# Kernel optimization log

Hardware: AMD Instinct MI355X
Metric: run time of the kernel (lower is better)

Reference implementation:

```python
import jax, jax.numpy as jnp
import numpy as np

HIDDEN = 768
NUM_HEADS = 12
HEAD_SIZE = HIDDEN // NUM_HEADS
LN_EPS = 1e-5


def setup_inputs() -> dict:
    key = jax.random.key(0)
    ks = jax.random.split(key, 10)
    B, S, H = 2, 4096, HIDDEN
    std = 1.0 / np.sqrt(H)
    inp = {
        "hidden_states": jax.random.normal(ks[0], (B, S, H), dtype=jnp.float32),
        "attention_mask": jnp.ones((B, S), dtype=jnp.float32),
        "Wq": jax.random.normal(ks[1], (H, H), dtype=jnp.float32) * std,
        "bq": jnp.zeros((H,), dtype=jnp.float32),
        "Wk": jax.random.normal(ks[2], (H, H), dtype=jnp.float32) * std,
        "bk": jnp.zeros((H,), dtype=jnp.float32),
        "Wv": jax.random.normal(ks[3], (H, H), dtype=jnp.float32) * std,
        "bv": jnp.zeros((H,), dtype=jnp.float32),
        "Wo": jax.random.normal(ks[4], (H, H), dtype=jnp.float32) * std,
        "bo": jnp.zeros((H,), dtype=jnp.float32),
        "ln_gamma": jnp.ones((H,), dtype=jnp.float32),
        "ln_beta": jnp.zeros((H,), dtype=jnp.float32),
    }
    return inp


def _split_heads(x):
    # [B, S, H] -> [B, nH, S, hd]
    B, S, _ = x.shape
    return x.reshape(B, S, NUM_HEADS, HEAD_SIZE).transpose(0, 2, 1, 3)


def reference(hidden_states, attention_mask, Wq, bq, Wk, bk, Wv, bv, Wo, bo, ln_gamma, ln_beta):
    # QKV projections (torch Linear: x @ W.T + b; here W is stored as [in, out])
    q = _split_heads(hidden_states @ Wq + bq)
    k = _split_heads(hidden_states @ Wk + bk)
    v = _split_heads(hidden_states @ Wv + bv)

    scores = jnp.einsum("bhqd,bhkd->bhqk", q, k) / jnp.sqrt(jnp.float32(HEAD_SIZE))
    # additive mask: (1 - mask) * -10000, broadcast over heads and query positions
    scores = scores + (1.0 - attention_mask)[:, None, None, :] * -10000.0
    probs = jax.nn.softmax(scores, axis=-1)  # dropout_prob = 0 -> identity

    ctx = jnp.einsum("bhqk,bhkd->bhqd", probs, v)
    B, _, S, _ = ctx.shape
    ctx = ctx.transpose(0, 2, 1, 3).reshape(B, S, HIDDEN)

    out = ctx @ Wo + bo
    resid = out + hidden_states
    mu = jnp.mean(resid, axis=-1, keepdims=True)
    var = jnp.var(resid, axis=-1, keepdims=True)
    return (resid - mu) * jax.lax.rsqrt(var + LN_EPS) * ln_gamma + ln_beta
```

## Files before the change

kernel.cpp:

```cpp
#include <hip/hip_runtime.h>
#include <hip/hip_bf16.h>

#define HID 768
#define NHEADS 12
#define HDIM 64
#define SEQ 4096
#define BB 2
#define MTOT (BB * SEQ)

typedef __attribute__((ext_vector_type(8))) short bf16x8;
typedef __attribute__((ext_vector_type(16))) float f32x16;

#define LOG2E 1.4426950408889634f

__device__ inline unsigned pack2bf(float a, float b) {
    __hip_bfloat162 h = __float22bfloat162_rn(float2{a, b});
    return *(unsigned*)&h;
}

__global__ __launch_bounds__(256) void cast_x_kernel(
    const float* __restrict__ X, __hip_bfloat16* __restrict__ Xb)
{
    const size_t i = ((size_t)blockIdx.x * 256 + threadIdx.x) * 8;
    const float4 x0 = *(const float4*)(X + i);
    const float4 x1 = *(const float4*)(X + i + 4);
    unsigned u[4];
    u[0] = pack2bf(x0.x, x0.y);
    u[1] = pack2bf(x0.z, x0.w);
    u[2] = pack2bf(x1.x, x1.y);
    u[3] = pack2bf(x1.z, x1.w);
    *(uint4*)(Xb + i) = *(uint4*)u;
}

__global__ __launch_bounds__(256) void pack_w_kernel(
    const float* __restrict__ Wq, const float* __restrict__ Wk,
    const float* __restrict__ Wv, const float* __restrict__ Wo,
    __hip_bfloat16* __restrict__ Wt)
{
    const int z = blockIdx.z;
    const float* __restrict__ W = (z == 0) ? Wq : (z == 1) ? Wk : (z == 2) ? Wv : Wo;
    const int in0  = blockIdx.x * 64;
    const int out0 = blockIdx.y * 64;
    const int t = threadIdx.x;

    __shared__ float T[64][65];
#pragma unroll
    for (int i = 0; i < 4; ++i) {
        const int idx = t + 256 * i;
        const int row = idx >> 4;
        const int c4  = (idx & 15) << 2;
        const float4 v = *(const float4*)(W + (size_t)(in0 + row) * HID + out0 + c4);
        T[row][c4 + 0] = v.x; T[row][c4 + 1] = v.y;
        T[row][c4 + 2] = v.z; T[row][c4 + 3] = v.w;
    }
    __syncthreads();

    const int o  = t >> 2;
    const int cb = (t & 3) << 4;
    __hip_bfloat16 tmp[16];
#pragma unroll
    for (int k = 0; k < 16; ++k)
        tmp[k] = __float2bfloat16(T[cb + k][o]);
    __hip_bfloat16* __restrict__ dst =
        Wt + (size_t)(z * HID + out0 + o) * HID + in0 + cb;
    *(uint4*)(dst)     = *(uint4*)(&tmp[0]);
    *(uint4*)(dst + 8) = *(uint4*)(&tmp[8]);
}

__global__ __launch_bounds__(256) void qkv_mfma_kernel(
    const __hip_bfloat16* __restrict__ Xb, const __hip_bfloat16* __restrict__ Wt,
    const float* __restrict__ bq, const float* __restrict__ bk,
    const float* __restrict__ bv,
    __hip_bfloat16* __restrict__ Qo, __hip_bfloat16* __restrict__ Ko,
    __hip_bfloat16* __restrict__ Vo)
{
    const int nblk = blockIdx.x;
    const int z  = nblk / 6;
    const int f0 = (nblk % 6) * 128;
    const int n0 = nblk * 128;
    const int m0 = blockIdx.y * 128;

    const float* __restrict__ bias = (z == 0) ? bq : (z == 1) ? bk : bv;

    const int t    = threadIdx.x;
    const int w    = t >> 6;
    const int lane = t & 63;
    const int col  = lane & 31;
    const int g    = lane >> 5;
    const int wm   = w & 1;
    const int wn   = w >> 1;

    __shared__ __hip_bfloat16 smem[2 * 128 * 72];
    __hip_bfloat16 (*As)[72] = (__hip_bfloat16(*)[72])smem;
    __hip_bfloat16 (*Bs)[72] = (__hip_bfloat16(*)[72])(smem + 128 * 72);

    f32x16 acc[2][2];
#pragma unroll
    for (int mt = 0; mt < 2; ++mt)
#pragma unroll
        for (int nt = 0; nt < 2; ++nt)
#pragma unroll
            for (int r = 0; r < 16; ++r) acc[mt][nt][r] = 0.f;

    for (int k0 = 0; k0 < HID; k0 += 64) {
        __syncthreads();
#pragma unroll
        for (int i = 0; i < 4; ++i) {
            const int idx = t + 256 * i;
            const int row = idx >> 3;
            const int c8  = (idx & 7) << 3;
            *(uint4*)&As[row][c8] = *(const uint4*)(Xb + (size_t)(m0 + row) * HID + k0 + c8);
            *(uint4*)&Bs[row][c8] = *(const uint4*)(Wt + (size_t)(n0 + row) * HID + k0 + c8);
        }
        __syncthreads();
#pragma unroll
        for (int kh = 0; kh < 4; ++kh) {
            const int ko = 16 * kh + 8 * g;
            const bf16x8 a0 = *(const bf16x8*)&As[64 * wm + col][ko];
            const bf16x8 a1 = *(const bf16x8*)&As[64 * wm + 32 + col][ko];
            const bf16x8 b0 = *(const bf16x8*)&Bs[64 * wn + col][ko];
            const bf16x8 b1 = *(const bf16x8*)&Bs[64 * wn + 32 + col][ko];
            acc[0][0] = __builtin_amdgcn_mfma_f32_32x32x16_bf16(a0, b0, acc[0][0], 0, 0, 0);
            acc[0][1] = __builtin_amdgcn_mfma_f32_32x32x16_bf16(a0, b1, acc[0][1], 0, 0, 0);
            acc[1][0] = __builtin_amdgcn_mfma_f32_32x32x16_bf16(a1, b0, acc[1][0], 0, 0, 0);
            acc[1][1] = __builtin_amdgcn_mfma_f32_32x32x16_bf16(a1, b1, acc[1][1], 0, 0, 0);
        }
    }

    if (z < 2) {
        __hip_bfloat16* __restrict__ Out = (z == 0) ? Qo : Ko;
        const int h = (f0 >> 6) + wn;
#pragma unroll
        for (int mt = 0; mt < 2; ++mt)
#pragma unroll
            for (int nt = 0; nt < 2; ++nt) {
                const int d = 32 * nt + col;
                const float bsv = bias[f0 + 64 * wn + d];
#pragma unroll
                for (int r = 0; r < 16; ++r) {
                    const int m = m0 + 64 * wm + 32 * mt + (r & 3) + 8 * (r >> 2) + 4 * g;
                    const int b = m >> 12;
                    const int s = m & (SEQ - 1);
                    Out[(((size_t)(b * NHEADS + h)) * SEQ + s) * HDIM + d] =
                        __float2bfloat16(acc[mt][nt][r] + bsv);
                }
            }
    } else {
        __syncthreads();
        __hip_bfloat16 (*Ts)[136] = (__hip_bfloat16(*)[136])smem;
#pragma unroll
        for (int mt = 0; mt < 2; ++mt)
#pragma unroll
            for (int nt = 0; nt < 2; ++nt) {
                const int nloc = 64 * wn + 32 * nt + col;
                const float bsv = bias[f0 + nloc];
#pragma unroll
                for (int rg = 0; rg < 4; ++rg) {
                    const int mbase = 64 * wm + 32 * mt + 8 * rg + 4 * g;
                    unsigned pu[2];
                    pu[0] = pack2bf(acc[mt][nt][4 * rg + 0] + bsv,
                                    acc[mt][nt][4 * rg + 1] + bsv);
                    pu[1] = pack2bf(acc[mt][nt][4 * rg + 2] + bsv,
                                    acc[mt][nt][4 * rg + 3] + bsv);
                    *(uint2*)&Ts[nloc][mbase] = *(uint2*)pu;
                }
            }
        __syncthreads();
        const int nloc = t >> 1;
        const int half = t & 1;
        const int hh = (f0 >> 6) + (nloc >> 6);
        const int d  = nloc & 63;
        const int bb = m0 >> 12;
        const int s0 = m0 & (SEQ - 1);
        __hip_bfloat16* __restrict__ dst =
            Vo + (((size_t)(bb * NHEADS + hh)) * HDIM + d) * SEQ + s0 + 64 * half;
        const __hip_bfloat16* srcp = &Ts[nloc][64 * half];
#pragma unroll
        for (int j = 0; j < 8; ++j)
            *(uint4*)(dst + 8 * j) = *(const uint4*)(srcp + 8 * j);
    }
}

__global__ __launch_bounds__(256, 3) void attn_kernel(
    const __hip_bfloat16* __restrict__ Qb, const __hip_bfloat16* __restrict__ Kb,
    const __hip_bfloat16* __restrict__ Vt, const float* __restrict__ mask,
    __hip_bfloat16* __restrict__ Op, float* __restrict__ lp)
{
    const int bh = blockIdx.y;
    const int b  = bh / NHEADS;
    const int h  = bh - b * NHEADS;
    const int kspan = SEQ / gridDim.z;
    const int kbeg  = blockIdx.z * kspan;

    const int t    = threadIdx.x;
    const int w    = t >> 6;
    const int lane = t & 63;
    const int col  = lane & 31;
    const int g    = lane >> 5;
    const int qw   = blockIdx.x * 128 + 32 * w;

    __shared__ __hip_bfloat16 Ks[128][72];
    __shared__ __hip_bfloat16 Vts[64][136];
    __shared__ float madd[128];

    const __hip_bfloat16* __restrict__ Qh = Qb + (size_t)bh * SEQ * HDIM;
    const __hip_bfloat16* __restrict__ Kh = Kb + (size_t)bh * SEQ * HDIM;
    const __hip_bfloat16* __restrict__ Vh = Vt + (size_t)bh * HDIM * SEQ;

    bf16x8 bq[4];
#pragma unroll
    for (int kh = 0; kh < 4; ++kh)
        bq[kh] = *(const bf16x8*)(Qh + (size_t)(qw + col) * HDIM + 16 * kh + 8 * g);

    f32x16 O[2];
    f32x16 ZERO;
    float lac = 0.f;
#pragma unroll
    for (int r = 0; r < 16; ++r) { O[0][r] = 0.f; O[1][r] = 0.f; ZERO[r] = 0.f; }

    const float kscale = 0.125f * LOG2E;

    for (int kt0 = 0; kt0 < kspan; kt0 += 128) {
        const int kt = kbeg + kt0;
        __syncthreads();
#pragma unroll
        for (int i = 0; i < 4; ++i) {
            const int idx = t + 256 * i;
            const int krow = idx >> 3;
            const int kc8  = (idx & 7) << 3;
            *(uint4*)&Ks[krow][kc8] = *(const uint4*)(Kh + (size_t)(kt + krow) * HDIM + kc8);
            const int vrow = idx >> 4;
            const int vc8  = (idx & 15) << 3;
            *(uint4*)&Vts[vrow][vc8] = *(const uint4*)(Vh + (size_t)vrow * SEQ + kt + vc8);
        }
        if (t < 128) madd[t] = (1.0f - mask[b * SEQ + kt + t]) * (-10000.0f * LOG2E);
        __syncthreads();

#pragma unroll
        for (int sub = 0; sub < 2; ++sub) {
            const int kb = 64 * sub;

            f32x16 St[2];
            {
                const bf16x8 ak0 = *(const bf16x8*)&Ks[kb + col][8 * g];
                const bf16x8 ak1 = *(const bf16x8*)&Ks[kb + 32 + col][8 * g];
                St[0] = __builtin_amdgcn_mfma_f32_32x32x16_bf16(ak0, bq[0], ZERO, 0, 0, 0);
                St[1] = __builtin_amdgcn_mfma_f32_32x32x16_bf16(ak1, bq[0], ZERO, 0, 0, 0);
            }
#pragma unroll
            for (int kh = 1; kh < 4; ++kh) {
                const bf16x8 ak0 = *(const bf16x8*)&Ks[kb + col][16 * kh + 8 * g];
                const bf16x8 ak1 = *(const bf16x8*)&Ks[kb + 32 + col][16 * kh + 8 * g];
                St[0] = __builtin_amdgcn_mfma_f32_32x32x16_bf16(ak0, bq[kh], St[0], 0, 0, 0);
                St[1] = __builtin_amdgcn_mfma_f32_32x32x16_bf16(ak1, bq[kh], St[1], 0, 0, 0);
            }

            unsigned g4x[2][4], g4y[2][4];
#pragma unroll
            for (int nt = 0; nt < 2; ++nt) {
#pragma unroll
                for (int b4 = 0; b4 < 4; ++b4) {
                    const float4 mm = *(const float4*)&madd[kb + 32 * nt + 8 * b4 + 4 * g];
                    const float p0 = __builtin_amdgcn_exp2f(fmaf(St[nt][4 * b4 + 0], kscale, mm.x));
                    const float p1 = __builtin_amdgcn_exp2f(fmaf(St[nt][4 * b4 + 1], kscale, mm.y));
                    const float p2 = __builtin_amdgcn_exp2f(fmaf(St[nt][4 * b4 + 2], kscale, mm.z));
                    const float p3 = __builtin_amdgcn_exp2f(fmaf(St[nt][4 * b4 + 3], kscale, mm.w));
                    lac += (p0 + p1) + (p2 + p3);
                    g4x[nt][b4] = pack2bf(p0, p1);
                    g4y[nt][b4] = pack2bf(p2, p3);
                }
            }

#pragma unroll
            for (int kh = 0; kh < 4; ++kh) {
                const int nt  = kh >> 1;
                const int khl = kh & 1;
                const unsigned lo_x = g4x[nt][2 * khl],     lo_y = g4y[nt][2 * khl];
                const unsigned hi_x = g4x[nt][2 * khl + 1], hi_y = g4y[nt][2 * khl + 1];
                const unsigned sx = g ? lo_x : hi_x;
                const unsigned sy = g ? lo_y : hi_y;
                const unsigned rx = (unsigned)__shfl_xor((int)sx, 32, 64);
                const unsigned ry = (unsigned)__shfl_xor((int)sy, 32, 64);
                union { unsigned u[4]; bf16x8 v; } au;
                if (g) { au.u[0] = rx; au.u[1] = ry; au.u[2] = hi_x; au.u[3] = hi_y; }
                else   { au.u[0] = lo_x; au.u[1] = lo_y; au.u[2] = rx; au.u[3] = ry; }
                const bf16x8 bv0 = *(const bf16x8*)&Vts[col][kb + 16 * kh + 8 * g];
                const bf16x8 bv1 = *(const bf16x8*)&Vts[32 + col][kb + 16 * kh + 8 * g];
                O[0] = __builtin_amdgcn_mfma_f32_32x32x16_bf16(au.v, bv0, O[0], 0, 0, 0);
                O[1] = __builtin_amdgcn_mfma_f32_32x32x16_bf16(au.v, bv1, O[1], 0, 0, 0);
            }
        }
    }

    const size_t opbase = (size_t)blockIdx.z * ((size_t)MTOT * HID);
    const float l = lac + __shfl_xor(lac, 32, 64);
    if (g == 0)
        lp[((size_t)blockIdx.z * (BB * NHEADS) + bh) * SEQ + qw + col] = l;
#pragma unroll
    for (int dt = 0; dt < 2; ++dt)
#pragma unroll
        for (int r = 0; r < 16; ++r) {
            const int q = qw + (r & 3) + 8 * (r >> 2) + 4 * g;
            const int d = 32 * dt + col;
            Op[opbase + ((size_t)b * SEQ + q) * HID + h * HDIM + d] =
                __float2bfloat16(O[dt][r]);
        }
}

__global__ __launch_bounds__(256) void combine_kernel(
    const __hip_bfloat16* __restrict__ Op, const float* __restrict__ lp,
    __hip_bfloat16* __restrict__ Ctx, int KS)
{
    const size_t i = ((size_t)blockIdx.x * 256 + threadIdx.x) * 8;
    const int n   = (int)(i % HID);
    const int row = (int)(i / HID);
    const int h = n >> 6;
    const int b = row >> 12;
    const int q = row & (SEQ - 1);
    const int bh = b * NHEADS + h;

    float denom = 0.f;
    float o[8] = {};
    for (int kz = 0; kz < KS; ++kz) {
        denom += lp[((size_t)kz * (BB * NHEADS) + bh) * SEQ + q];
        uint4 u = *(const uint4*)(Op + (size_t)kz * ((size_t)MTOT * HID) + i);
        const __hip_bfloat16* e = (const __hip_bfloat16*)&u;
#pragma unroll
        for (int j = 0; j < 8; ++j) o[j] += __bfloat162float(e[j]);
    }
    const float inv = 1.0f / denom;
    unsigned u[4];
#pragma unroll
    for (int j = 0; j < 4; ++j)
        u[j] = pack2bf(o[2 * j] * inv, o[2 * j + 1] * inv);
    *(uint4*)(Ctx + i) = *(uint4*)u;
}

__global__ __launch_bounds__(256) void out_mfma_kernel(
    const __hip_bfloat16* __restrict__ Cb, const __hip_bfloat16* __restrict__ Wto,
    const float* __restrict__ bo, const float* __restrict__ X,
    float* __restrict__ Resid)
{
    const int n0 = blockIdx.x * 128;
    const int m0 = blockIdx.y * 128;

    const int t    = threadIdx.x;
    const int w    = t >> 6;
    const int lane = t & 63;
    const int col  = lane & 31;
    const int g    = lane >> 5;
    const int wm   = w & 1;
    const int wn   = w >> 1;

    __shared__ __hip_bfloat16 As[128][72];
    __shared__ __hip_bfloat16 Bs[128][72];

    f32x16 acc[2][2];
#pragma unroll
    for (int mt = 0; mt < 2; ++mt)
#pragma unroll
        for (int nt = 0; nt < 2; ++nt)
#pragma unroll
            for (int r = 0; r < 16; ++r) acc[mt][nt][r] = 0.f;

    for (int k0 = 0; k0 < HID; k0 += 64) {
        __syncthreads();
#pragma unroll
        for (int i = 0; i < 4; ++i) {
            const int idx = t + 256 * i;
            const int row = idx >> 3;
            const int c8  = (idx & 7) << 3;
            *(uint4*)&As[row][c8] = *(const uint4*)(Cb  + (size_t)(m0 + row) * HID + k0 + c8);
            *(uint4*)&Bs[row][c8] = *(const uint4*)(Wto + (size_t)(n0 + row) * HID + k0 + c8);
        }
        __syncthreads();
#pragma unroll
        for (int kh = 0; kh < 4; ++kh) {
            const int ko = 16 * kh + 8 * g;
            const bf16x8 a0 = *(const bf16x8*)&As[64 * wm + col][ko];
            const bf16x8 a1 = *(const bf16x8*)&As[64 * wm + 32 + col][ko];
            const bf16x8 b0 = *(const bf16x8*)&Bs[64 * wn + col][ko];
            const bf16x8 b1 = *(const bf16x8*)&Bs[64 * wn + 32 + col][ko];
            acc[0][0] = __builtin_amdgcn_mfma_f32_32x32x16_bf16(a0, b0, acc[0][0], 0, 0, 0);
            acc[0][1] = __builtin_amdgcn_mfma_f32_32x32x16_bf16(a0, b1, acc[0][1], 0, 0, 0);
            acc[1][0] = __builtin_amdgcn_mfma_f32_32x32x16_bf16(a1, b0, acc[1][0], 0, 0, 0);
            acc[1][1] = __builtin_amdgcn_mfma_f32_32x32x16_bf16(a1, b1, acc[1][1], 0, 0, 0);
        }
    }

#pragma unroll
    for (int mt = 0; mt < 2; ++mt)
#pragma unroll
        for (int nt = 0; nt < 2; ++nt) {
            const int n = n0 + 64 * wn + 32 * nt + col;
            const float bsv = bo[n];
#pragma unroll
            for (int r = 0; r < 16; ++r) {
                const int m = m0 + 64 * wm + 32 * mt + (r & 3) + 8 * (r >> 2) + 4 * g;
                Resid[(size_t)m * HID + n] = acc[mt][nt][r] + bsv + X[(size_t)m * HID + n];
            }
        }
}

__global__ __launch_bounds__(256) void ln_kernel(
    const float* __restrict__ Rin, const float* __restrict__ gamma,
    const float* __restrict__ beta, float* __restrict__ Out)
{
    const int row = blockIdx.x;
    const int t   = threadIdx.x;
    const float* __restrict__ x = Rin + (size_t)row * HID;

    const float v0 = x[t];
    const float v1 = x[t + 256];
    const float v2 = x[t + 512];
    float s  = v0 + v1 + v2;
    float s2 = v0 * v0 + v1 * v1 + v2 * v2;
#pragma unroll
    for (int off = 32; off; off >>= 1) {
        s  += __shfl_xor(s,  off, 64);
        s2 += __shfl_xor(s2, off, 64);
    }
    __shared__ float rs[4], rs2[4];
    const int w = t >> 6, lane = t & 63;
    if (lane == 0) { rs[w] = s; rs2[w] = s2; }
    __syncthreads();
    const float tot  = rs[0] + rs[1] + rs[2] + rs[3];
    const float tot2 = rs2[0] + rs2[1] + rs2[2] + rs2[3];
    const float mu   = tot * (1.0f / HID);
    const float var  = tot2 * (1.0f / HID) - mu * mu;
    const float rsig = rsqrtf(var + 1e-5f);

    float* __restrict__ y = Out + (size_t)row * HID;
    y[t]       = (v0 - mu) * rsig * gamma[t]       + beta[t];
    y[t + 256] = (v1 - mu) * rsig * gamma[t + 256] + beta[t + 256];
    y[t + 512] = (v2 - mu) * rsig * gamma[t + 512] + beta[t + 512];
}

extern "C" void kernel_launch(void* const* d_in, const int* in_sizes, int n_in,
                              void* d_out, int out_size, void* d_ws, size_t ws_size,
                              hipStream_t stream)
{
    const float* X     = (const float*)d_in[0];
    const float* mask  = (const float*)d_in[1];
    const float* Wq    = (const float*)d_in[2];
    const float* bq    = (const float*)d_in[3];
    const float* Wk    = (const float*)d_in[4];
    const float* bk    = (const float*)d_in[5];
    const float* Wv    = (const float*)d_in[6];
    const float* bv    = (const float*)d_in[7];
    const float* Wo    = (const float*)d_in[8];
    const float* bo    = (const float*)d_in[9];
    const float* gamma = (const float*)d_in[10];
    const float* beta  = (const float*)d_in[11];
    float* out = (float*)d_out;

    const size_t N = (size_t)MTOT * HID;
    const size_t WTE = (size_t)4 * HID * HID;

    char* p = (char*)d_ws;
    __hip_bfloat16* Xb  = (__hip_bfloat16*)p;  p += 2 * N;
    __hip_bfloat16* Wt  = (__hip_bfloat16*)p;  p += 2 * WTE;
    __hip_bfloat16* Qw  = (__hip_bfloat16*)p;  p += 2 * N;
    __hip_bfloat16* Kw  = (__hip_bfloat16*)p;  p += 2 * N;
    __hip_bfloat16* Vtw = (__hip_bfloat16*)p;  p += 2 * N;
    char* opb = p;
    const size_t fixed = (size_t)(opb - (char*)d_ws);

    const size_t lpsz4 = 4 * (size_t)(BB * NHEADS) * SEQ * sizeof(float);
    const int KS = (ws_size >= fixed + 4 * 2 * N + lpsz4) ? 4 : 2;

    __hip_bfloat16* Op  = (__hip_bfloat16*)opb;
    float* lpt = (float*)(opb + (size_t)KS * 2 * N);
    __hip_bfloat16* Ctxb = Xb;
    float* Rd = (float*)Kw;

    cast_x_kernel<<<(int)(N / 2048), 256, 0, stream>>>(X, Xb);
    pack_w_kernel<<<dim3(12, 12, 4), 256, 0, stream>>>(Wq, Wk, Wv, Wo, Wt);
    qkv_mfma_kernel<<<dim3(18, MTOT / 128), 256, 0, stream>>>(
        Xb, Wt, bq, bk, bv, Qw, Kw, Vtw);
    attn_kernel<<<dim3(SEQ / 128, BB * NHEADS, KS), 256, 0, stream>>>(
        Qw, Kw, Vtw, mask, Op, lpt);
    combine_kernel<<<(int)(N / 2048), 256, 0, stream>>>(Op, lpt, Ctxb, KS);
    out_mfma_kernel<<<dim3(6, MTOT / 128), 256, 0, stream>>>(
        Ctxb, Wt + (size_t)2304 * HID, bo, X, Rd);
    ln_kernel<<<MTOT, 256, 0, stream>>>(Rd, gamma, beta, out);
}
```

Measured before the change: 337.8 us.

## Drop split-K attention partials and fuse softmax normalization into attention

The attention kernel now walks all keys per block instead of splitting the key range across grid.z. It normalizes the output by the row sum in-kernel, staging the sums in shared memory, and writes the bf16 context directly. This removes the partial-output buffers and the separate combine kernel, which saves a large amount of global memory traffic and one launch. The X cast and weight pack kernels are also merged into one launch. The cost is fewer attention blocks (768), each with a longer serial loop, so parallelism and latency hiding drop.

```diff
diff --git a/kernel.cpp b/kernel.cpp
--- a/kernel.cpp
+++ b/kernel.cpp
@@ -18,30 +18,34 @@
     return *(unsigned*)&h;
 }
 
-__global__ __launch_bounds__(256) void cast_x_kernel(
-    const float* __restrict__ X, __hip_bfloat16* __restrict__ Xb)
-{
-    const size_t i = ((size_t)blockIdx.x * 256 + threadIdx.x) * 8;
-    const float4 x0 = *(const float4*)(X + i);
-    const float4 x1 = *(const float4*)(X + i + 4);
-    unsigned u[4];
-    u[0] = pack2bf(x0.x, x0.y);
-    u[1] = pack2bf(x0.z, x0.w);
-    u[2] = pack2bf(x1.x, x1.y);
-    u[3] = pack2bf(x1.z, x1.w);
-    *(uint4*)(Xb + i) = *(uint4*)u;
-}
-
-__global__ __launch_bounds__(256) void pack_w_kernel(
+__global__ __launch_bounds__(256) void prep_kernel(
+    const float* __restrict__ X, __hip_bfloat16* __restrict__ Xb,
     const float* __restrict__ Wq, const float* __restrict__ Wk,
     const float* __restrict__ Wv, const float* __restrict__ Wo,
     __hip_bfloat16* __restrict__ Wt)
 {
-    const int z = blockIdx.z;
+    const int blk = blockIdx.x;
+    const int t = threadIdx.x;
+
+    if (blk < 3072) {
+        const size_t i = ((size_t)blk * 256 + t) * 8;
+        const float4 x0 = *(const float4*)(X + i);
+        const float4 x1 = *(const float4*)(X + i + 4);
+        unsigned u[4];
+        u[0] = pack2bf(x0.x, x0.y);
+        u[1] = pack2bf(x0.z, x0.w);
+        u[2] = pack2bf(x1.x, x1.y);
+        u[3] = pack2bf(x1.z, x1.w);
+        *(uint4*)(Xb + i) = *(uint4*)u;
+        return;
+    }
+
+    const int pb = blk - 3072;
+    const int z  = pb / 144;
+    const int rem = pb - z * 144;
+    const int in0  = (rem % 12) * 64;
+    const int out0 = (rem / 12) * 64;
     const float* __restrict__ W = (z == 0) ? Wq : (z == 1) ? Wk : (z == 2) ? Wv : Wo;
-    const int in0  = blockIdx.x * 64;
-    const int out0 = blockIdx.y * 64;
-    const int t = threadIdx.x;
 
     __shared__ float T[64][65];
 #pragma unroll
@@ -184,13 +188,11 @@
 __global__ __launch_bounds__(256, 3) void attn_kernel(
     const __hip_bfloat16* __restrict__ Qb, const __hip_bfloat16* __restrict__ Kb,
     const __hip_bfloat16* __restrict__ Vt, const float* __restrict__ mask,
-    __hip_bfloat16* __restrict__ Op, float* __restrict__ lp)
+    __hip_bfloat16* __restrict__ Ctx)
 {
     const int bh = blockIdx.y;
     const int b  = bh / NHEADS;
     const int h  = bh - b * NHEADS;
-    const int kspan = SEQ / gridDim.z;
-    const int kbeg  = blockIdx.z * kspan;
 
     const int t    = threadIdx.x;
     const int w    = t >> 6;
@@ -202,6 +204,7 @@
     __shared__ __hip_bfloat16 Ks[128][72];
     __shared__ __hip_bfloat16 Vts[64][136];
     __shared__ float madd[128];
+    __shared__ float lw[4][32];
 
     const __hip_bfloat16* __restrict__ Qh = Qb + (size_t)bh * SEQ * HDIM;
     const __hip_bfloat16* __restrict__ Kh = Kb + (size_t)bh * SEQ * HDIM;
@@ -220,8 +223,7 @@
 
     const float kscale = 0.125f * LOG2E;
 
-    for (int kt0 = 0; kt0 < kspan; kt0 += 128) {
-        const int kt = kbeg + kt0;
+    for (int kt = 0; kt < SEQ; kt += 128) {
         __syncthreads();
 #pragma unroll
         for (int i = 0; i < 4; ++i) {
@@ -292,48 +294,20 @@
         }
     }
 
-    const size_t opbase = (size_t)blockIdx.z * ((size_t)MTOT * HID);
     const float l = lac + __shfl_xor(lac, 32, 64);
-    if (g == 0)
-        lp[((size_t)blockIdx.z * (BB * NHEADS) + bh) * SEQ + qw + col] = l;
-#pragma unroll
-    for (int dt = 0; dt < 2; ++dt)
-#pragma unroll
-        for (int r = 0; r < 16; ++r) {
-            const int q = qw + (r & 3) + 8 * (r >> 2) + 4 * g;
-            const int d = 32 * dt + col;
-            Op[opbase + ((size_t)b * SEQ + q) * HID + h * HDIM + d] =
-                __float2bfloat16(O[dt][r]);
-        }
-}
-
-__global__ __launch_bounds__(256) void combine_kernel(
-    const __hip_bfloat16* __restrict__ Op, const float* __restrict__ lp,
-    __hip_bfloat16* __restrict__ Ctx, int KS)
-{
-    const size_t i = ((size_t)blockIdx.x * 256 + threadIdx.x) * 8;
-    const int n   = (int)(i % HID);
-    const int row = (int)(i / HID);
-    const int h = n >> 6;
-    const int b = row >> 12;
-    const int q = row & (SEQ - 1);
-    const int bh = b * NHEADS + h;
-
-    float denom = 0.f;
-    float o[8] = {};
-    for (int kz = 0; kz < KS; ++kz) {
-        denom += lp[((size_t)kz * (BB * NHEADS) + bh) * SEQ + q];
-        uint4 u = *(const uint4*)(Op + (size_t)kz * ((size_t)MTOT * HID) + i);
-        const __hip_bfloat16* e = (const __hip_bfloat16*)&u;
-#pragma unroll
-        for (int j = 0; j < 8; ++j) o[j] += __bfloat162float(e[j]);
-    }
-    const float inv = 1.0f / denom;
-    unsigned u[4];
-#pragma unroll
-    for (int j = 0; j < 4; ++j)
-        u[j] = pack2bf(o[2 * j] * inv, o[2 * j + 1] * inv);
-    *(uint4*)(Ctx + i) = *(uint4*)u;
+    __syncthreads();
+    if (g == 0) lw[w][col] = l;
+    __syncthreads();
+
+#pragma unroll
+    for (int r = 0; r < 16; ++r) {
+        const int qloc = (r & 3) + 8 * (r >> 2) + 4 * g;
+        const float linv = 1.0f / lw[w][qloc];
+        const int q = qw + qloc;
+        const size_t base = ((size_t)b * SEQ + q) * HID + h * HDIM;
+        Ctx[base + col]      = __float2bfloat16(O[0][r] * linv);
+        Ctx[base + 32 + col] = __float2bfloat16(O[1][r] * linv);
+    }
 }
 
 __global__ __launch_bounds__(256) void out_mfma_kernel(
@@ -463,24 +437,15 @@
     __hip_bfloat16* Qw  = (__hip_bfloat16*)p;  p += 2 * N;
     __hip_bfloat16* Kw  = (__hip_bfloat16*)p;  p += 2 * N;
     __hip_bfloat16* Vtw = (__hip_bfloat16*)p;  p += 2 * N;
-    char* opb = p;
-    const size_t fixed = (size_t)(opb - (char*)d_ws);
-
-    const size_t lpsz4 = 4 * (size_t)(BB * NHEADS) * SEQ * sizeof(float);
-    const int KS = (ws_size >= fixed + 4 * 2 * N + lpsz4) ? 4 : 2;
-
-    __hip_bfloat16* Op  = (__hip_bfloat16*)opb;
-    float* lpt = (float*)(opb + (size_t)KS * 2 * N);
+
     __hip_bfloat16* Ctxb = Xb;
     float* Rd = (float*)Kw;
 
-    cast_x_kernel<<<(int)(N / 2048), 256, 0, stream>>>(X, Xb);
-    pack_w_kernel<<<dim3(12, 12, 4), 256, 0, stream>>>(Wq, Wk, Wv, Wo, Wt);
+    prep_kernel<<<3648, 256, 0, stream>>>(X, Xb, Wq, Wk, Wv, Wo, Wt);
     qkv_mfma_kernel<<<dim3(18, MTOT / 128), 256, 0, stream>>>(
         Xb, Wt, bq, bk, bv, Qw, Kw, Vtw);
-    attn_kernel<<<dim3(SEQ / 128, BB * NHEADS, KS), 256, 0, stream>>>(
-        Qw, Kw, Vtw, mask, Op, lpt);
-    combine_kernel<<<(int)(N / 2048), 256, 0, stream>>>(Op, lpt, Ctxb, KS);
+    attn_kernel<<<dim3(SEQ / 128, BB * NHEADS), 256, 0, stream>>>(
+        Qw, Kw, Vtw, mask, Ctxb);
     out_mfma_kernel<<<dim3(6, MTOT / 128), 256, 0, stream>>>(
         Ctxb, Wt + (size_t)2304 * HID, bo, X, Rd);
     ln_kernel<<<MTOT, 256, 0, stream>>>(Rd, gamma, beta, out);
```

Result: no change. 336.0 us (-0.5%).
